# Optimization experiments

Measured on AMD Instinct MI355X. Metric: run time of the kernel, lower is better.

The kernel has to match this reference:

```python
import jax, jax.numpy as jnp
import numpy as np
from jax import lax

B, L, C = 4, 4096, 512
H = 8           # head_num
D = C // H      # head dim = 64
RR = 4          # reduction_ratio -> reducer conv kernel 7, stride 4
KS = 3          # MixFFN depthwise kernel
ER = 4          # expansion ratio -> 2048 channels
EPS = 1e-5      # torch LayerNorm default eps


def _ln(x, g, b):
    # LayerNorm over last axis, affine per-channel
    m = jnp.mean(x, axis=-1, keepdims=True)
    v = jnp.mean(jnp.square(x - m), axis=-1, keepdims=True)
    return (x - m) * lax.rsqrt(v + EPS) * g + b


def setup_inputs() -> dict:
    key = jax.random.key(0)
    ks = jax.random.split(key, 9)
    s = lambda fan: 1.0 / np.sqrt(fan)
    return {
        "x": jax.random.normal(ks[0], (B, L, C), jnp.float32),
        "w_q": jax.random.normal(ks[1], (C, C), jnp.float32) * s(C),
        "w_k": jax.random.normal(ks[2], (C, C), jnp.float32) * s(C),
        "w_v": jax.random.normal(ks[3], (C, C), jnp.float32) * s(C),
        "w_o": jax.random.normal(ks[4], (C, C), jnp.float32) * s(C),
        "w_red": jax.random.normal(ks[5], (C, C, 2 * RR - 1), jnp.float32) * s(C * (2 * RR - 1)),
        "w_ffn1": jax.random.normal(ks[6], (C, C), jnp.float32) * s(C),
        "w_ffn_dw": jax.random.normal(ks[7], (C * ER, 1, KS), jnp.float32) * s(KS),
        "w_ffn2": jax.random.normal(ks[8], (C, C * ER), jnp.float32) * s(C * ER),
        "ln_gamma": jnp.ones((6, C), jnp.float32),
        "ln_beta": jnp.zeros((6, C), jnp.float32),
    }


def reference(x, w_q, w_k, w_v, w_o, w_red, w_ffn1, w_ffn_dw, w_ffn2, ln_gamma, ln_beta):
    # ln indices: 0=ln1(pre-attn), 1=ln(reducer), 2=ln_q, 3=ln_k, 4=ln_v, 5=ln2(pre-ffn)
    residual = x
    h = _ln(x, ln_gamma[0], ln_beta[0])  # B L C

    # --- spatial-reduction for K/V: reflect-pad strided conv + LN ---
    p = (2 * RR - 1) // 2
    hr = jnp.transpose(h, (0, 2, 1))  # B C L
    hr = jnp.pad(hr, ((0, 0), (0, 0), (p, p)), mode="reflect")
    red = lax.conv_general_dilated(hr, w_red, window_strides=(RR,), padding="VALID",
                                   dimension_numbers=("NCH", "OIH", "NCH"))  # B C Lr
    red = jnp.transpose(red, (0, 2, 1))  # B Lr C
    red = _ln(red, ln_gamma[1], ln_beta[1])

    # --- QKV projections + LayerNorms ---
    q = _ln(h @ w_q.T, ln_gamma[2], ln_beta[2])      # B L C
    k = _ln(red @ w_k.T, ln_gamma[3], ln_beta[3])    # B Lr C
    v = _ln(red @ w_v.T, ln_gamma[4], ln_beta[4])    # B Lr C

    Lr = k.shape[1]
    q = q.reshape(B, L, H, D).transpose(0, 2, 1, 3)   # B h L d
    k = k.reshape(B, Lr, H, D).transpose(0, 2, 1, 3)  # B h Lr d
    v = v.reshape(B, Lr, H, D).transpose(0, 2, 1, 3)

    scores = jnp.einsum("bhqd,bhkd->bhqk", q, k) / jnp.sqrt(jnp.float32(D))
    attn = jax.nn.softmax(scores, axis=-1)
    out = jnp.einsum("bhqk,bhkd->bhqd", attn, v)
    out = out.transpose(0, 2, 1, 3).reshape(B, L, C)
    out = out @ w_o.T

    h2 = out + residual
    residual2 = h2
    f = _ln(h2, ln_gamma[5], ln_beta[5])  # B L C

    # --- MixFFN: 1x1 conv -> depthwise reflect conv (groups=C, out=ER*C) -> GELU -> 1x1 conv ---
    f = jnp.transpose(f, (0, 2, 1))  # B C L
    f = jnp.einsum("oi,bil->bol", w_ffn1, f)  # 1x1, C->C
    pk = (KS - 1) // 2
    fp = jnp.pad(f, ((0, 0), (0, 0), (pk, pk)), mode="reflect")
    f = lax.conv_general_dilated(fp, w_ffn_dw, window_strides=(1,), padding="VALID",
                                 dimension_numbers=("NCH", "OIH", "NCH"),
                                 feature_group_count=C)  # B (ER*C) L
    f = jax.nn.gelu(f, approximate=False)  # torch nn.GELU() is exact erf
    f = jnp.einsum("oi,bil->bol", w_ffn2, f)  # 1x1, ER*C->C
    f = jnp.transpose(f, (0, 2, 1))  # B L C

    return f + residual2
```

## Files before the change

kernel.cpp:

```cpp
#include <hip/hip_runtime.h>
#include <math.h>

typedef __attribute__((ext_vector_type(8))) short short8;
typedef __attribute__((ext_vector_type(4))) float f32x4;
typedef unsigned short u16;
typedef unsigned int u32;
typedef unsigned long long u64;

namespace {
constexpr int kB = 4;
constexpr int kL = 4096;
constexpr int kC = 512;
constexpr int kH = 8;
constexpr int kLr = 1024;
constexpr int kCH = 2048;
constexpr int kKred = 3584;
constexpr float kEps = 1e-5f;
}

#define WAIT_VM(n) asm volatile("s_waitcnt vmcnt(" #n ")" ::: "memory")
#define WAIT_LGKM0 asm volatile("s_waitcnt lgkmcnt(0)" ::: "memory")
#define BARRIER_SB() do { __builtin_amdgcn_s_barrier(); __builtin_amdgcn_sched_barrier(0); } while (0)

__device__ __forceinline__ float bf2f(u16 u) { return __uint_as_float(((u32)u) << 16); }
__device__ __forceinline__ u16 f2bf(float f) {
  u32 u = __float_as_uint(f);
  u32 r = (u + 0x7fffu + ((u >> 16) & 1u)) >> 16;
  return (u16)r;
}
__device__ __forceinline__ u32 cvtpk(float lo, float hi) {
  u32 r;
  asm("v_cvt_pk_bf16_f32 %0, %1, %2" : "=v"(r) : "v"(lo), "v"(hi));
  return r;
}

__device__ __forceinline__ void gload_lds16(const void* g, void* l) {
  __builtin_amdgcn_global_load_lds(
      (const __attribute__((address_space(1))) unsigned int*)g,
      (__attribute__((address_space(3))) unsigned int*)l, 16, 0, 0);
}

__device__ __forceinline__ short8 ldsfrag(const u16* base, int row, int col16) {
  return *(const short8*)(base + (size_t)(((row << 3) + (col16 ^ (row & 7))) << 3));
}

__global__ __launch_bounds__(256) void cvt_weights_kernel(
    const float* __restrict__ w_q, const float* __restrict__ w_k,
    const float* __restrict__ w_v, const float* __restrict__ w_o,
    const float* __restrict__ w_f1, const float* __restrict__ w_f2,
    u16* __restrict__ dst) {
  const int i = (blockIdx.x * 256 + threadIdx.x) * 4;
  const int seg = i >> 18;
  const float* src;
  int off;
  if (seg < 5) {
    src = (seg == 0) ? w_q : (seg == 1) ? w_k : (seg == 2) ? w_v : (seg == 3) ? w_o : w_f1;
    off = i & 262143;
  } else {
    src = w_f2;
    off = i - 1310720;
  }
  const float4 v = *(const float4*)(src + off);
  u16 o[4] = {f2bf(v.x), f2bf(v.y), f2bf(v.z), f2bf(v.w)};
  *(u64*)(dst + i) = *(u64*)o;
}

__global__ __launch_bounds__(256) void repack_wred_kernel(const float* __restrict__ src,
                                                          u16* __restrict__ dst) {
  const int idx = blockIdx.x * 256 + threadIdx.x;
  if (idx >= kC * kKred) return;
  const int o = idx / kKred;
  const int rem = idx - o * kKred;
  const int t = rem >> 9;
  const int i = rem & (kC - 1);
  dst[idx] = f2bf(src[(size_t)(o * kC + i) * 7 + t]);
}

__global__ __launch_bounds__(256) void ln_bf16_kernel(const float* __restrict__ in,
                                                      u16* __restrict__ out,
                                                      const float* __restrict__ g,
                                                      const float* __restrict__ be) {
  const int row = blockIdx.x;
  const int tid = threadIdx.x;
  const float2 v = *(const float2*)(in + (size_t)row * kC + tid * 2);
  float s = v.x + v.y;
  float ss = v.x * v.x + v.y * v.y;
#pragma unroll
  for (int off = 32; off > 0; off >>= 1) {
    s += __shfl_down(s, off);
    ss += __shfl_down(ss, off);
  }
  __shared__ float wsum[4][2];
  __shared__ float mi[2];
  const int wave = tid >> 6, lane = tid & 63;
  if (lane == 0) { wsum[wave][0] = s; wsum[wave][1] = ss; }
  __syncthreads();
  if (tid == 0) {
    const float S = wsum[0][0] + wsum[1][0] + wsum[2][0] + wsum[3][0];
    const float SS = wsum[0][1] + wsum[1][1] + wsum[2][1] + wsum[3][1];
    const float mean = S * (1.0f / kC);
    const float var = SS * (1.0f / kC) - mean * mean;
    mi[0] = mean;
    mi[1] = rsqrtf(var + kEps);
  }
  __syncthreads();
  const float mean = mi[0], inv = mi[1];
  const float2 gg = *(const float2*)(g + tid * 2);
  const float2 bb = *(const float2*)(be + tid * 2);
  u16 o2[2] = {f2bf((v.x - mean) * inv * gg.x + bb.x), f2bf((v.y - mean) * inv * gg.y + bb.y)};
  *(u32*)(out + (size_t)row * kC + tid * 2) = *(u32*)o2;
}

__global__ __launch_bounds__(256) void reduce2_ln_kernel(const float* __restrict__ P,
                                                         u16* __restrict__ out,
                                                         const float* __restrict__ g,
                                                         const float* __restrict__ be) {
  const int row = blockIdx.x;
  const int tid = threadIdx.x;
  const size_t stride = (size_t)kB * kLr * kC;
  float2 v = make_float2(0.f, 0.f);
#pragma unroll
  for (int z = 0; z < 2; ++z) {
    const float2 p = *(const float2*)(P + z * stride + (size_t)row * kC + tid * 2);
    v.x += p.x;
    v.y += p.y;
  }
  float s = v.x + v.y;
  float ss = v.x * v.x + v.y * v.y;
#pragma unroll
  for (int off = 32; off > 0; off >>= 1) {
    s += __shfl_down(s, off);
    ss += __shfl_down(ss, off);
  }
  __shared__ float wsum[4][2];
  __shared__ float mi[2];
  const int wave = tid >> 6, lane = tid & 63;
  if (lane == 0) { wsum[wave][0] = s; wsum[wave][1] = ss; }
  __syncthreads();
  if (tid == 0) {
    const float S = wsum[0][0] + wsum[1][0] + wsum[2][0] + wsum[3][0];
    const float SS = wsum[0][1] + wsum[1][1] + wsum[2][1] + wsum[3][1];
    const float mean = S * (1.0f / kC);
    const float var = SS * (1.0f / kC) - mean * mean;
    mi[0] = mean;
    mi[1] = rsqrtf(var + kEps);
  }
  __syncthreads();
  const float mean = mi[0], inv = mi[1];
  const float2 gg = *(const float2*)(g + tid * 2);
  const float2 bb = *(const float2*)(be + tid * 2);
  u16 o2[2] = {f2bf((v.x - mean) * inv * gg.x + bb.x), f2bf((v.y - mean) * inv * gg.y + bb.y)};
  *(u32*)(out + (size_t)row * kC + tid * 2) = *(u32*)o2;
}

__global__ __launch_bounds__(256) void dwgelu_kernel(const u16* __restrict__ f1,
                                                     const float* __restrict__ wdw,
                                                     u16* __restrict__ fdw) {
  const int row = blockIdx.x;
  const int l = row & (kL - 1);
  const int rb = row - l;
  const int cc0 = threadIdx.x * 8;
  const int cg = cc0 >> 2;
  const int lm = (l == 0) ? 1 : l - 1;
  const int lp = (l == kL - 1) ? kL - 2 : l + 1;
  const u32 xm = *(const u32*)(f1 + (size_t)(rb + lm) * kC + cg);
  const u32 x0 = *(const u32*)(f1 + (size_t)(rb + l) * kC + cg);
  const u32 xp = *(const u32*)(f1 + (size_t)(rb + lp) * kC + cg);
  const float xml = bf2f((u16)xm), xmh = bf2f((u16)(xm >> 16));
  const float x0l = bf2f((u16)x0), x0h = bf2f((u16)(x0 >> 16));
  const float xpl = bf2f((u16)xp), xph = bf2f((u16)(xp >> 16));
  float wv[24];
#pragma unroll
  for (int t = 0; t < 6; ++t)
    *(float4*)&wv[t * 4] = *(const float4*)(wdw + (size_t)cc0 * 3 + t * 4);
  short8 pk;
#pragma unroll
  for (int j = 0; j < 8; ++j) {
    const float a_ = (j < 4) ? xml : xmh;
    const float b_ = (j < 4) ? x0l : x0h;
    const float c_ = (j < 4) ? xpl : xph;
    const float dw = wv[j * 3] * a_ + wv[j * 3 + 1] * b_ + wv[j * 3 + 2] * c_;
    pk[j] = (short)f2bf(0.5f * dw * (1.0f + erff(dw * 0.70710678118654752440f)));
  }
  *(short8*)(fdw + (size_t)row * kCH + cc0) = pk;
}

__global__ __launch_bounds__(256) void mgemm_red_kernel(
    const u16* __restrict__ A, const u16* __restrict__ W, float* __restrict__ OutF,
    int M, int N, int K) {
  __shared__ __align__(16) u16 As[2][128 * 64];
  __shared__ __align__(16) u16 Bs[2][128 * 64];
  const int tid = threadIdx.x;
  const int lane = tid & 63, w = tid >> 6;
  const int m0 = blockIdx.y * 128, n0 = blockIdx.x * 128;
  const int wm = (w >> 1) * 64, wn = (w & 1) * 64;
  const f32x4 zero = {0.f, 0.f, 0.f, 0.f};
  f32x4 acc[4][4];
#pragma unroll
  for (int i = 0; i < 4; ++i)
#pragma unroll
    for (int j = 0; j < 4; ++j) acc[i][j] = zero;

  const int kc = K / gridDim.z;
  const int kBeg = blockIdx.z * kc;
  float* outp = OutF + (size_t)blockIdx.z * M * N;

  auto stage = [&](int buf, int k0) {
#pragma unroll
    for (int c = 0; c < 4; ++c) {
      const int ci = w * 4 + c;
      const int idx = ci * 64 + lane;
      const int row = idx >> 3, s = idx & 7;
      const int c16 = s ^ (row & 7);
      gload_lds16(W + (size_t)(n0 + row) * K + k0 + c16 * 8, (char*)Bs[buf] + ci * 1024);
      const int m = m0 + row;
      const int b = m >> 10, lr = m & (kLr - 1);
      const int k = k0 + c16 * 8;
      const int t = k >> 9, i = k & (kC - 1);
      int pos = 4 * lr + t - 3;
      pos = pos < 0 ? -pos : (pos >= kL ? 2 * kL - 2 - pos : pos);
      gload_lds16(A + ((size_t)(b << 12) + pos) * kC + i, (char*)As[buf] + ci * 1024);
    }
  };

  const int nk = kc >> 6;
  stage(0, kBeg);
  stage(1, kBeg + 64);
  for (int t = 0; t < nk; ++t) {
    const int cur = t & 1;
    if (t + 1 < nk) WAIT_VM(8); else WAIT_VM(0);
    BARRIER_SB();
#pragma unroll
    for (int kst = 0; kst < 2; ++kst) {
      short8 af[4], bfr[4];
      const int c16 = kst * 4 + (lane >> 4);
#pragma unroll
      for (int mb = 0; mb < 4; ++mb) af[mb] = ldsfrag(As[cur], wm + mb * 16 + (lane & 15), c16);
#pragma unroll
      for (int nb = 0; nb < 4; ++nb) bfr[nb] = ldsfrag(Bs[cur], wn + nb * 16 + (lane & 15), c16);
#pragma unroll
      for (int mb = 0; mb < 4; ++mb)
#pragma unroll
        for (int nb = 0; nb < 4; ++nb)
          acc[mb][nb] = __builtin_amdgcn_mfma_f32_16x16x32_bf16(af[mb], bfr[nb], acc[mb][nb], 0, 0, 0);
    }
    WAIT_LGKM0;
    BARRIER_SB();
    if (t + 2 < nk) stage(cur, kBeg + ((t + 2) << 6));
  }
#pragma unroll
  for (int mb = 0; mb < 4; ++mb)
#pragma unroll
    for (int r = 0; r < 4; ++r) {
      const int row = m0 + wm + mb * 16 + ((lane >> 4) << 2) + r;
#pragma unroll
      for (int nb = 0; nb < 4; ++nb)
        outp[(size_t)row * N + n0 + wn + nb * 16 + (lane & 15)] = acc[mb][nb][r];
    }
}

__global__ __launch_bounds__(256) void mgemm_res_kernel(
    const u16* __restrict__ A, const u16* __restrict__ W,
    const float* __restrict__ Res, float* __restrict__ OutF, int M, int N, int K) {
  __shared__ __align__(16) u16 As[2][128 * 64];
  __shared__ __align__(16) u16 Bs[2][128 * 64];
  const int tid = threadIdx.x;
  const int lane = tid & 63, w = tid >> 6;
  const int m0 = blockIdx.y * 128, n0 = blockIdx.x * 128;
  const int wm = (w >> 1) * 64, wn = (w & 1) * 64;
  const f32x4 zero = {0.f, 0.f, 0.f, 0.f};
  f32x4 acc[4][4];
#pragma unroll
  for (int i = 0; i < 4; ++i)
#pragma unroll
    for (int j = 0; j < 4; ++j) acc[i][j] = zero;

  auto stage = [&](int buf, int k0) {
#pragma unroll
    for (int c = 0; c < 4; ++c) {
      const int ci = w * 4 + c;
      const int idx = ci * 64 + lane;
      const int row = idx >> 3, s = idx & 7;
      const int c16 = s ^ (row & 7);
      gload_lds16(W + (size_t)(n0 + row) * K + k0 + c16 * 8, (char*)Bs[buf] + ci * 1024);
      gload_lds16(A + (size_t)(m0 + row) * K + k0 + c16 * 8, (char*)As[buf] + ci * 1024);
    }
  };

  const int nk = K >> 6;
  stage(0, 0);
  stage(1, 64);
  for (int t = 0; t < nk; ++t) {
    const int cur = t & 1;
    if (t + 1 < nk) WAIT_VM(8); else WAIT_VM(0);
    BARRIER_SB();
#pragma unroll
    for (int kst = 0; kst < 2; ++kst) {
      short8 af[4], bfr[4];
      const int c16 = kst * 4 + (lane >> 4);
#pragma unroll
      for (int mb = 0; mb < 4; ++mb) af[mb] = ldsfrag(As[cur], wm + mb * 16 + (lane & 15), c16);
#pragma unroll
      for (int nb = 0; nb < 4; ++nb) bfr[nb] = ldsfrag(Bs[cur], wn + nb * 16 + (lane & 15), c16);
#pragma unroll
      for (int mb = 0; mb < 4; ++mb)
#pragma unroll
        for (int nb = 0; nb < 4; ++nb)
          acc[mb][nb] = __builtin_amdgcn_mfma_f32_16x16x32_bf16(af[mb], bfr[nb], acc[mb][nb], 0, 0, 0);
    }
    WAIT_LGKM0;
    BARRIER_SB();
    if (t + 2 < nk) stage(cur, (t + 2) << 6);
  }
#pragma unroll
  for (int mb = 0; mb < 4; ++mb)
#pragma unroll
    for (int r = 0; r < 4; ++r) {
      const int row = m0 + wm + mb * 16 + ((lane >> 4) << 2) + r;
#pragma unroll
      for (int nb = 0; nb < 4; ++nb) {
        const size_t off = (size_t)row * N + n0 + wn + nb * 16 + (lane & 15);
        OutF[off] = acc[mb][nb][r] + Res[off];
      }
    }
}

template <int EPI>
__global__ __launch_bounds__(512) void gemm512_kernel(
    const u16* __restrict__ A, const u16* __restrict__ W,
    const float* __restrict__ Res, float* __restrict__ OutF,
    u16* __restrict__ OutB, u16* __restrict__ OutB2,
    int K, const float* __restrict__ gam, const float* __restrict__ bet, float oscale) {
  constexpr bool RES_ = (EPI == 3);
  constexpr bool LN_ = (EPI == 1 || EPI == 2 || EPI == 3);
  __shared__ __align__(16) u16 As[2][64 * 64];
  __shared__ __align__(16) u16 Bs[2][512 * 64];
  const int tid = threadIdx.x;
  const int lane = tid & 63, w = tid >> 6;
  const int l15 = lane & 15, g = lane >> 4;
  const int m0 = blockIdx.y * 64;
  const int n0 = blockIdx.x * 512;
  const int wn = w << 6;
  const f32x4 zero = {0.f, 0.f, 0.f, 0.f};
  f32x4 acc[4][4];
#pragma unroll
  for (int i = 0; i < 4; ++i)
#pragma unroll
    for (int j = 0; j < 4; ++j) acc[i][j] = zero;

  auto stage = [&](int buf, int k0) {
#pragma unroll
    for (int c = 0; c < 8; ++c) {
      const int cg = (w << 3) + c;
      const int idx = (cg << 6) + lane;
      const int row = idx >> 3, sl = idx & 7;
      const int c16 = sl ^ (row & 7);
      gload_lds16(W + (size_t)(n0 + row) * K + k0 + (c16 << 3), (char*)Bs[buf] + cg * 1024);
    }
    const int idx = (w << 6) + lane;
    const int row = idx >> 3, sl = idx & 7;
    const int c16 = sl ^ (row & 7);
    gload_lds16(A + (size_t)(m0 + row) * K + k0 + (c16 << 3), (char*)As[buf] + w * 1024);
  };

  const int nk = K >> 6;
  stage(0, 0);
  stage(1, 64);
  for (int t = 0; t < nk; ++t) {
    const int cur = t & 1;
    if (t + 1 < nk) WAIT_VM(9); else WAIT_VM(0);
    BARRIER_SB();
#pragma unroll
    for (int kst = 0; kst < 2; ++kst) {
      const int c16 = (kst << 2) + g;
      short8 af[4], bfr[4];
#pragma unroll
      for (int mb = 0; mb < 4; ++mb) af[mb] = ldsfrag(As[cur], (mb << 4) + l15, c16);
#pragma unroll
      for (int nb = 0; nb < 4; ++nb) bfr[nb] = ldsfrag(Bs[cur], wn + (nb << 4) + l15, c16);
#pragma unroll
      for (int mb = 0; mb < 4; ++mb)
#pragma unroll
        for (int nb = 0; nb < 4; ++nb)
          acc[mb][nb] = __builtin_amdgcn_mfma_f32_16x16x32_bf16(af[mb], bfr[nb], acc[mb][nb], 0, 0, 0);
    }
    WAIT_LGKM0;
    BARRIER_SB();
    if (t + 2 < nk) stage(cur, (t + 2) << 6);
  }

  if (RES_) {
#pragma unroll
    for (int mb = 0; mb < 4; ++mb)
#pragma unroll
      for (int r = 0; r < 4; ++r) {
        const int grow = m0 + (mb << 4) + (g << 2) + r;
#pragma unroll
        for (int nb = 0; nb < 4; ++nb)
          acc[mb][nb][r] += Res[(size_t)grow * kC + wn + (nb << 4) + l15];
      }
  }
  float* rs = (float*)As[0];
  float* rs2 = rs + 512;
  float2* minv = (float2*)(rs2 + 512);
  if (LN_) {
#pragma unroll
    for (int mb = 0; mb < 4; ++mb)
#pragma unroll
      for (int r = 0; r < 4; ++r) {
        float s = acc[mb][0][r] + acc[mb][1][r] + acc[mb][2][r] + acc[mb][3][r];
        float s2 = acc[mb][0][r] * acc[mb][0][r] + acc[mb][1][r] * acc[mb][1][r] +
                   acc[mb][2][r] * acc[mb][2][r] + acc[mb][3][r] * acc[mb][3][r];
        s += __shfl_xor(s, 1); s += __shfl_xor(s, 2); s += __shfl_xor(s, 4); s += __shfl_xor(s, 8);
        s2 += __shfl_xor(s2, 1); s2 += __shfl_xor(s2, 2); s2 += __shfl_xor(s2, 4); s2 += __shfl_xor(s2, 8);
        if (l15 == 0) {
          const int row = (mb << 4) + (g << 2) + r;
          rs[(w << 6) + row] = s;
          rs2[(w << 6) + row] = s2;
        }
      }
    __syncthreads();
    if (tid < 64) {
      float S = 0.f, SS = 0.f;
#pragma unroll
      for (int w8 = 0; w8 < 8; ++w8) { S += rs[(w8 << 6) + tid]; SS += rs2[(w8 << 6) + tid]; }
      const float mean = S * (1.0f / 512.0f);
      const float var = SS * (1.0f / 512.0f) - mean * mean;
      minv[tid] = make_float2(mean, rsqrtf(var + kEps));
    }
    __syncthreads();
  }
  float g4[4], b4[4];
  if (LN_) {
    const float* gp = (EPI == 2 && blockIdx.x) ? gam + kC : gam;
    const float* bp = (EPI == 2 && blockIdx.x) ? bet + kC : bet;
#pragma unroll
    for (int nb = 0; nb < 4; ++nb) {
      const int cc = wn + (nb << 4) + l15;
      g4[nb] = gp[cc];
      b4[nb] = bp[cc];
    }
  }
#pragma unroll
  for (int mb = 0; mb < 4; ++mb) {
#pragma unroll
    for (int r = 0; r < 4; ++r) {
      const int row = (mb << 4) + (g << 2) + r;
      const int grow = m0 + row;
      float2 mi = make_float2(0.f, 0.f);
      if (LN_) mi = minv[row];
#pragma unroll
      for (int nb = 0; nb < 4; ++nb) {
        const int cc = wn + (nb << 4) + l15;
        const float vv = acc[mb][nb][r];
        if (EPI == 0) {
          OutB[(size_t)grow * kC + cc] = f2bf(vv);
        } else if (EPI == 1) {
          OutB[(size_t)grow * kC + cc] = f2bf(((vv - mi.x) * mi.y * g4[nb] + b4[nb]) * oscale);
        } else if (EPI == 2) {
          const float lv = (vv - mi.x) * mi.y * g4[nb] + b4[nb];
          if (blockIdx.x == 0) {
            OutB[(size_t)grow * kC + cc] = f2bf(lv);
          } else {
            const int b = grow >> 10, lr = grow & (kLr - 1);
            const int hh = cc >> 6, d = cc & 63;
            OutB2[((size_t)((b << 3) + hh) * 64 + d) * kLr + lr] = f2bf(lv);
          }
        } else {
          OutF[(size_t)grow * kC + cc] = vv;
          OutB[(size_t)grow * kC + cc] = f2bf((vv - mi.x) * mi.y * g4[nb] + b4[nb]);
        }
      }
    }
  }
}

__global__ __launch_bounds__(256) void attn_mfma_kernel(
    const u16* __restrict__ q, const u16* __restrict__ k,
    const u16* __restrict__ vt, u16* __restrict__ o) {
  __shared__ __align__(16) u16 Ks[2][64 * 64];
  __shared__ __align__(16) u16 Vs[2][64 * 64];
  __shared__ __align__(16) u16 Ps[4][16 * 64];
  const int tid = threadIdx.x;
  const int lane = tid & 63, w = tid >> 6;
  const int qt = blockIdx.x, h = blockIdx.y, b = blockIdx.z;
  const int q0 = qt << 6;
  const int l15 = lane & 15, g = lane >> 4;

  short8 qf[2];
#pragma unroll
  for (int kst = 0; kst < 2; ++kst)
    qf[kst] = *(const short8*)(q + (size_t)((b << 12) + q0 + (w << 4) + l15) * kC +
                               (h << 6) + kst * 32 + g * 8);

  auto stageKV = [&](int buf, int t) {
    const int kv0 = t << 6;
#pragma unroll
    for (int c = 0; c < 2; ++c) {
      const int ci = (w << 1) + c;
      const int a16 = (ci << 6) + lane;
      const int r = a16 >> 3, sl = a16 & 7;
      const int c16 = sl ^ (r & 7);
      gload_lds16(k + (size_t)((b << 10) + kv0 + r) * kC + (h << 6) + (c16 << 3),
                  (char*)Ks[buf] + ci * 1024);
      gload_lds16(vt + (size_t)(((b << 3) + h) * 64 + r) * kLr + kv0 + (c16 << 3),
                  (char*)Vs[buf] + ci * 1024);
    }
  };

  stageKV(0, 0);
  stageKV(1, 1);

  const f32x4 zero = {0.f, 0.f, 0.f, 0.f};
  float m1 = -1e30f, l1 = 0.f;
  f32x4 accO[4] = {zero, zero, zero, zero};
  constexpr int nt = kLr / 64;

  for (int t = 0; t < nt; ++t) {
    const int cur = t & 1;
    if (t + 1 < nt) WAIT_VM(4); else WAIT_VM(0);
    BARRIER_SB();
    f32x4 st[4] = {zero, zero, zero, zero};
    __builtin_amdgcn_s_setprio(1);
#pragma unroll
    for (int kst = 0; kst < 2; ++kst) {
      const int c16 = (kst << 2) + g;
#pragma unroll
      for (int nb = 0; nb < 4; ++nb) {
        const short8 ak = ldsfrag(Ks[cur], (nb << 4) + l15, c16);
        st[nb] = __builtin_amdgcn_mfma_f32_16x16x32_bf16(ak, qf[kst], st[nb], 0, 0, 0);
      }
    }
    __builtin_amdgcn_s_setprio(0);
    {
      float pm = -1e30f;
#pragma unroll
      for (int nb = 0; nb < 4; ++nb)
#pragma unroll
        for (int r = 0; r < 4; ++r) pm = fmaxf(pm, st[nb][r]);
      pm = fmaxf(pm, __shfl_xor(pm, 16));
      pm = fmaxf(pm, __shfl_xor(pm, 32));
      const bool sk = __all(pm - m1 <= 11.5f);
      float scl = 1.0f;
      if (!sk) {
        const float mnew = fmaxf(m1, pm);
        scl = exp2f(m1 - mnew);
        m1 = mnew;
      }
      float ps = 0.f;
#pragma unroll
      for (int nb = 0; nb < 4; ++nb)
#pragma unroll
        for (int r = 0; r < 4; ++r) {
          const float e = exp2f(st[nb][r] - m1);
          st[nb][r] = e;
          ps += e;
        }
      ps += __shfl_xor(ps, 16);
      ps += __shfl_xor(ps, 32);
      l1 = l1 * scl + ps;
      char* pw = (char*)&Ps[w][0];
#pragma unroll
      for (int nb = 0; nb < 4; ++nb) {
        const u32 lo = cvtpk(st[nb][0], st[nb][1]);
        const u32 hi = cvtpk(st[nb][2], st[nb][3]);
        const int slot = ((nb << 1) + (g >> 1)) ^ (l15 & 7);
        *(u64*)(pw + (l15 << 7) + (slot << 4) + ((g & 1) << 3)) = ((u64)hi << 32) | lo;
      }
      if (!sk) {
        float scA[4];
#pragma unroll
        for (int r = 0; r < 4; ++r) scA[r] = __shfl(scl, (g << 2) + r);
#pragma unroll
        for (int d = 0; d < 4; ++d)
#pragma unroll
          for (int r = 0; r < 4; ++r) accO[d][r] *= scA[r];
      }
    }
    __builtin_amdgcn_s_setprio(1);
#pragma unroll
    for (int kvs = 0; kvs < 2; ++kvs) {
      const int c16 = (kvs << 2) + g;
      const short8 ap = ldsfrag(&Ps[w][0], l15, c16);
#pragma unroll
      for (int d = 0; d < 4; ++d) {
        const short8 bv = ldsfrag(Vs[cur], (d << 4) + l15, c16);
        accO[d] = __builtin_amdgcn_mfma_f32_16x16x32_bf16(ap, bv, accO[d], 0, 0, 0);
      }
    }
    __builtin_amdgcn_s_setprio(0);
    WAIT_LGKM0;
    BARRIER_SB();
    if (t + 2 < nt) stageKV(cur, t + 2);
  }
  float li[4];
#pragma unroll
  for (int r = 0; r < 4; ++r) li[r] = 1.0f / __shfl(l1, (g << 2) + r);
  const int qg = (b << 12) + q0 + (w << 4) + (g << 2);
#pragma unroll
  for (int d = 0; d < 4; ++d)
#pragma unroll
    for (int r = 0; r < 4; ++r)
      o[(size_t)(qg + r) * kC + (h << 6) + (d << 4) + l15] = f2bf(accO[d][r] * li[r]);
}

extern "C" void kernel_launch(void* const* d_in, const int* in_sizes, int n_in,
                              void* d_out, int out_size, void* d_ws, size_t ws_size,
                              hipStream_t stream) {
  const float* x      = (const float*)d_in[0];
  const float* w_q    = (const float*)d_in[1];
  const float* w_k    = (const float*)d_in[2];
  const float* w_v    = (const float*)d_in[3];
  const float* w_o    = (const float*)d_in[4];
  const float* w_red  = (const float*)d_in[5];
  const float* w_ffn1 = (const float*)d_in[6];
  const float* w_dw   = (const float*)d_in[7];
  const float* w_ffn2 = (const float*)d_in[8];
  const float* gam    = (const float*)d_in[9];
  const float* bet    = (const float*)d_in[10];
  float* out = (float*)d_out;

  const size_t nBLC = (size_t)kB * kL * kC;
  const size_t nBLrC = (size_t)kB * kLr * kC;
  u16* us = (u16*)d_ws;
  u16* wqb   = us;
  u16* wkb   = wqb + 262144;
  u16* wob   = wkb + 2 * 262144;
  u16* wf1b  = wob + 262144;
  u16* wf2b  = wf1b + 262144;
  u16* wredb = wf2b + 1048576;
  u16* h_b   = wredb + 1835008;
  u16* q_b   = h_b + nBLC;
  u16* red_b = q_b + nBLC;
  u16* k_b   = red_b + nBLrC;
  u16* vt_b  = k_b + nBLrC;
  float* S   = (float*)(vt_b + nBLrC);
  u16* fdw   = q_b;

  cvt_weights_kernel<<<2304, 256, 0, stream>>>(w_q, w_k, w_v, w_o, w_ffn1, w_ffn2, wqb);
  repack_wred_kernel<<<7168, 256, 0, stream>>>(w_red, wredb);

  ln_bf16_kernel<<<kB * kL, 256, 0, stream>>>(x, h_b, gam, bet);
  mgemm_red_kernel<<<dim3(4, 32, 2), 256, 0, stream>>>(h_b, wredb, S, kB * kLr, kC, kKred);
  reduce2_ln_kernel<<<kB * kLr, 256, 0, stream>>>(S, red_b, gam + kC, bet + kC);
  gemm512_kernel<1><<<dim3(1, 256), 512, 0, stream>>>(
      h_b, wqb, nullptr, nullptr, q_b, nullptr, kC, gam + 2 * kC, bet + 2 * kC,
      0.125f * 1.44269504088896f);
  gemm512_kernel<2><<<dim3(2, 64), 512, 0, stream>>>(
      red_b, wkb, nullptr, nullptr, k_b, vt_b, kC, gam + 3 * kC, bet + 3 * kC, 1.0f);
  attn_mfma_kernel<<<dim3(kL / 64, kH, kB), 256, 0, stream>>>(q_b, k_b, vt_b, h_b);
  gemm512_kernel<3><<<dim3(1, 256), 512, 0, stream>>>(
      h_b, wob, x, out, q_b, nullptr, kC, gam + 5 * kC, bet + 5 * kC, 1.0f);
  gemm512_kernel<0><<<dim3(1, 256), 512, 0, stream>>>(
      q_b, wf1b, nullptr, nullptr, h_b, nullptr, kC, nullptr, nullptr, 1.0f);
  dwgelu_kernel<<<kB * kL, 256, 0, stream>>>(h_b, w_dw, fdw);
  mgemm_res_kernel<<<dim3(4, 128), 256, 0, stream>>>(fdw, wf2b, out, out, kB * kL, kC, kCH);
}
```

Measured before the change: 319.8 us.

## Switch GEMM and attention kernels to 1024-thread blocks with single-stage prefetch

Replaces the explicit vmcnt-based two-stage prefetch with a simpler scheme: issue the next tile's loads, compute the current one, then __syncthreads. The 512-wide GEMM now uses 16 waves, splitting M across two wave rows, which halves per-wave accumulators. Attention grows to 16 waves and 256 queries per block, with K and V loads split across wave groups. This trades explicit wait control and prefetch depth for more waves per block and higher occupancy. The __syncthreads waits for all outstanding loads each step, so load latency may be less well hidden.

```diff
diff --git a/kernel.cpp b/kernel.cpp
--- a/kernel.cpp
+++ b/kernel.cpp
@@ -17,10 +17,6 @@
 constexpr int kKred = 3584;
 constexpr float kEps = 1e-5f;
 }
-
-#define WAIT_VM(n) asm volatile("s_waitcnt vmcnt(" #n ")" ::: "memory")
-#define WAIT_LGKM0 asm volatile("s_waitcnt lgkmcnt(0)" ::: "memory")
-#define BARRIER_SB() do { __builtin_amdgcn_s_barrier(); __builtin_amdgcn_sched_barrier(0); } while (0)
 
 __device__ __forceinline__ float bf2f(u16 u) { return __uint_as_float(((u32)u) << 16); }
 __device__ __forceinline__ u16 f2bf(float f) {
@@ -225,11 +221,10 @@
 
   const int nk = kc >> 6;
   stage(0, kBeg);
-  stage(1, kBeg + 64);
+  __syncthreads();
   for (int t = 0; t < nk; ++t) {
     const int cur = t & 1;
-    if (t + 1 < nk) WAIT_VM(8); else WAIT_VM(0);
-    BARRIER_SB();
+    if (t + 1 < nk) stage(cur ^ 1, kBeg + ((t + 1) << 6));
 #pragma unroll
     for (int kst = 0; kst < 2; ++kst) {
       short8 af[4], bfr[4];
@@ -244,9 +239,7 @@
         for (int nb = 0; nb < 4; ++nb)
           acc[mb][nb] = __builtin_amdgcn_mfma_f32_16x16x32_bf16(af[mb], bfr[nb], acc[mb][nb], 0, 0, 0);
     }
-    WAIT_LGKM0;
-    BARRIER_SB();
-    if (t + 2 < nk) stage(cur, kBeg + ((t + 2) << 6));
+    __syncthreads();
   }
 #pragma unroll
   for (int mb = 0; mb < 4; ++mb)
@@ -289,11 +282,10 @@
 
   const int nk = K >> 6;
   stage(0, 0);
-  stage(1, 64);
+  __syncthreads();
   for (int t = 0; t < nk; ++t) {
     const int cur = t & 1;
-    if (t + 1 < nk) WAIT_VM(8); else WAIT_VM(0);
-    BARRIER_SB();
+    if (t + 1 < nk) stage(cur ^ 1, (t + 1) << 6);
 #pragma unroll
     for (int kst = 0; kst < 2; ++kst) {
       short8 af[4], bfr[4];
@@ -308,9 +300,7 @@
         for (int nb = 0; nb < 4; ++nb)
           acc[mb][nb] = __builtin_amdgcn_mfma_f32_16x16x32_bf16(af[mb], bfr[nb], acc[mb][nb], 0, 0, 0);
     }
-    WAIT_LGKM0;
-    BARRIER_SB();
-    if (t + 2 < nk) stage(cur, (t + 2) << 6);
+    __syncthreads();
   }
 #pragma unroll
   for (int mb = 0; mb < 4; ++mb)
@@ -326,7 +316,7 @@
 }
 
 template <int EPI>
-__global__ __launch_bounds__(512) void gemm512_kernel(
+__global__ __launch_bounds__(1024) void gemm512_kernel(
     const u16* __restrict__ A, const u16* __restrict__ W,
     const float* __restrict__ Res, float* __restrict__ OutF,
     u16* __restrict__ OutB, u16* __restrict__ OutB2,
@@ -340,61 +330,61 @@
   const int l15 = lane & 15, g = lane >> 4;
   const int m0 = blockIdx.y * 64;
   const int n0 = blockIdx.x * 512;
-  const int wn = w << 6;
+  const int wm = (w >> 3) << 5;
+  const int wn = (w & 7) << 6;
   const f32x4 zero = {0.f, 0.f, 0.f, 0.f};
-  f32x4 acc[4][4];
-#pragma unroll
-  for (int i = 0; i < 4; ++i)
+  f32x4 acc[2][4];
+#pragma unroll
+  for (int i = 0; i < 2; ++i)
 #pragma unroll
     for (int j = 0; j < 4; ++j) acc[i][j] = zero;
 
   auto stage = [&](int buf, int k0) {
 #pragma unroll
-    for (int c = 0; c < 8; ++c) {
-      const int cg = (w << 3) + c;
+    for (int c = 0; c < 4; ++c) {
+      const int cg = (w << 2) + c;
       const int idx = (cg << 6) + lane;
       const int row = idx >> 3, sl = idx & 7;
       const int c16 = sl ^ (row & 7);
       gload_lds16(W + (size_t)(n0 + row) * K + k0 + (c16 << 3), (char*)Bs[buf] + cg * 1024);
     }
-    const int idx = (w << 6) + lane;
-    const int row = idx >> 3, sl = idx & 7;
-    const int c16 = sl ^ (row & 7);
-    gload_lds16(A + (size_t)(m0 + row) * K + k0 + (c16 << 3), (char*)As[buf] + w * 1024);
+    if (w < 8) {
+      const int idx = (w << 6) + lane;
+      const int row = idx >> 3, sl = idx & 7;
+      const int c16 = sl ^ (row & 7);
+      gload_lds16(A + (size_t)(m0 + row) * K + k0 + (c16 << 3), (char*)As[buf] + w * 1024);
+    }
   };
 
   const int nk = K >> 6;
   stage(0, 0);
-  stage(1, 64);
+  __syncthreads();
   for (int t = 0; t < nk; ++t) {
     const int cur = t & 1;
-    if (t + 1 < nk) WAIT_VM(9); else WAIT_VM(0);
-    BARRIER_SB();
+    if (t + 1 < nk) stage(cur ^ 1, (t + 1) << 6);
 #pragma unroll
     for (int kst = 0; kst < 2; ++kst) {
       const int c16 = (kst << 2) + g;
-      short8 af[4], bfr[4];
-#pragma unroll
-      for (int mb = 0; mb < 4; ++mb) af[mb] = ldsfrag(As[cur], (mb << 4) + l15, c16);
+      short8 af[2], bfr[4];
+#pragma unroll
+      for (int mb = 0; mb < 2; ++mb) af[mb] = ldsfrag(As[cur], wm + (mb << 4) + l15, c16);
 #pragma unroll
       for (int nb = 0; nb < 4; ++nb) bfr[nb] = ldsfrag(Bs[cur], wn + (nb << 4) + l15, c16);
 #pragma unroll
-      for (int mb = 0; mb < 4; ++mb)
+      for (int mb = 0; mb < 2; ++mb)
 #pragma unroll
         for (int nb = 0; nb < 4; ++nb)
           acc[mb][nb] = __builtin_amdgcn_mfma_f32_16x16x32_bf16(af[mb], bfr[nb], acc[mb][nb], 0, 0, 0);
     }
-    WAIT_LGKM0;
-    BARRIER_SB();
-    if (t + 2 < nk) stage(cur, (t + 2) << 6);
+    __syncthreads();
   }
 
   if (RES_) {
 #pragma unroll
-    for (int mb = 0; mb < 4; ++mb)
+    for (int mb = 0; mb < 2; ++mb)
 #pragma unroll
       for (int r = 0; r < 4; ++r) {
-        const int grow = m0 + (mb << 4) + (g << 2) + r;
+        const int grow = m0 + wm + (mb << 4) + (g << 2) + r;
 #pragma unroll
         for (int nb = 0; nb < 4; ++nb)
           acc[mb][nb][r] += Res[(size_t)grow * kC + wn + (nb << 4) + l15];
@@ -405,7 +395,7 @@
   float2* minv = (float2*)(rs2 + 512);
   if (LN_) {
 #pragma unroll
-    for (int mb = 0; mb < 4; ++mb)
+    for (int mb = 0; mb < 2; ++mb)
 #pragma unroll
       for (int r = 0; r < 4; ++r) {
         float s = acc[mb][0][r] + acc[mb][1][r] + acc[mb][2][r] + acc[mb][3][r];
@@ -414,16 +404,16 @@
         s += __shfl_xor(s, 1); s += __shfl_xor(s, 2); s += __shfl_xor(s, 4); s += __shfl_xor(s, 8);
         s2 += __shfl_xor(s2, 1); s2 += __shfl_xor(s2, 2); s2 += __shfl_xor(s2, 4); s2 += __shfl_xor(s2, 8);
         if (l15 == 0) {
-          const int row = (mb << 4) + (g << 2) + r;
-          rs[(w << 6) + row] = s;
-          rs2[(w << 6) + row] = s2;
+          const int rowf = wm + (mb << 4) + (g << 2) + r;
+          rs[((w & 7) << 6) + rowf] = s;
+          rs2[((w & 7) << 6) + rowf] = s2;
         }
       }
     __syncthreads();
     if (tid < 64) {
       float S = 0.f, SS = 0.f;
 #pragma unroll
-      for (int w8 = 0; w8 < 8; ++w8) { S += rs[(w8 << 6) + tid]; SS += rs2[(w8 << 6) + tid]; }
+      for (int c8 = 0; c8 < 8; ++c8) { S += rs[(c8 << 6) + tid]; SS += rs2[(c8 << 6) + tid]; }
       const float mean = S * (1.0f / 512.0f);
       const float var = SS * (1.0f / 512.0f) - mean * mean;
       minv[tid] = make_float2(mean, rsqrtf(var + kEps));
@@ -442,13 +432,13 @@
     }
   }
 #pragma unroll
-  for (int mb = 0; mb < 4; ++mb) {
+  for (int mb = 0; mb < 2; ++mb) {
 #pragma unroll
     for (int r = 0; r < 4; ++r) {
-      const int row = (mb << 4) + (g << 2) + r;
-      const int grow = m0 + row;
+      const int rowf = wm + (mb << 4) + (g << 2) + r;
+      const int grow = m0 + rowf;
       float2 mi = make_float2(0.f, 0.f);
-      if (LN_) mi = minv[row];
+      if (LN_) mi = minv[rowf];
 #pragma unroll
       for (int nb = 0; nb < 4; ++nb) {
         const int cc = wn + (nb << 4) + l15;
@@ -475,16 +465,16 @@
   }
 }
 
-__global__ __launch_bounds__(256) void attn_mfma_kernel(
+__global__ __launch_bounds__(1024) void attn_mfma_kernel(
     const u16* __restrict__ q, const u16* __restrict__ k,
     const u16* __restrict__ vt, u16* __restrict__ o) {
   __shared__ __align__(16) u16 Ks[2][64 * 64];
   __shared__ __align__(16) u16 Vs[2][64 * 64];
-  __shared__ __align__(16) u16 Ps[4][16 * 64];
+  __shared__ __align__(16) u16 Ps[16][16 * 64];
   const int tid = threadIdx.x;
   const int lane = tid & 63, w = tid >> 6;
   const int qt = blockIdx.x, h = blockIdx.y, b = blockIdx.z;
-  const int q0 = qt << 6;
+  const int q0 = qt << 8;
   const int l15 = lane & 15, g = lane >> 4;
 
   short8 qf[2];
@@ -495,31 +485,30 @@
 
   auto stageKV = [&](int buf, int t) {
     const int kv0 = t << 6;
-#pragma unroll
-    for (int c = 0; c < 2; ++c) {
-      const int ci = (w << 1) + c;
-      const int a16 = (ci << 6) + lane;
-      const int r = a16 >> 3, sl = a16 & 7;
-      const int c16 = sl ^ (r & 7);
+    const int ci = w & 7;
+    const int a16 = (ci << 6) + lane;
+    const int r = a16 >> 3, sl = a16 & 7;
+    const int c16 = sl ^ (r & 7);
+    if (w < 8)
       gload_lds16(k + (size_t)((b << 10) + kv0 + r) * kC + (h << 6) + (c16 << 3),
                   (char*)Ks[buf] + ci * 1024);
+    else
       gload_lds16(vt + (size_t)(((b << 3) + h) * 64 + r) * kLr + kv0 + (c16 << 3),
                   (char*)Vs[buf] + ci * 1024);
-    }
   };
 
   stageKV(0, 0);
-  stageKV(1, 1);
 
   const f32x4 zero = {0.f, 0.f, 0.f, 0.f};
   float m1 = -1e30f, l1 = 0.f;
   f32x4 accO[4] = {zero, zero, zero, zero};
   constexpr int nt = kLr / 64;
 
+  __syncthreads();
+
   for (int t = 0; t < nt; ++t) {
     const int cur = t & 1;
-    if (t + 1 < nt) WAIT_VM(4); else WAIT_VM(0);
-    BARRIER_SB();
+    if (t + 1 < nt) stageKV(cur ^ 1, t + 1);
     f32x4 st[4] = {zero, zero, zero, zero};
     __builtin_amdgcn_s_setprio(1);
 #pragma unroll
@@ -589,9 +578,7 @@
       }
     }
     __builtin_amdgcn_s_setprio(0);
-    WAIT_LGKM0;
-    BARRIER_SB();
-    if (t + 2 < nt) stageKV(cur, t + 2);
+    __syncthreads();
   }
   float li[4];
 #pragma unroll
@@ -643,15 +630,15 @@
   ln_bf16_kernel<<<kB * kL, 256, 0, stream>>>(x, h_b, gam, bet);
   mgemm_red_kernel<<<dim3(4, 32, 2), 256, 0, stream>>>(h_b, wredb, S, kB * kLr, kC, kKred);
   reduce2_ln_kernel<<<kB * kLr, 256, 0, stream>>>(S, red_b, gam + kC, bet + kC);
-  gemm512_kernel<1><<<dim3(1, 256), 512, 0, stream>>>(
+  gemm512_kernel<1><<<dim3(1, 256), 1024, 0, stream>>>(
       h_b, wqb, nullptr, nullptr, q_b, nullptr, kC, gam + 2 * kC, bet + 2 * kC,
       0.125f * 1.44269504088896f);
-  gemm512_kernel<2><<<dim3(2, 64), 512, 0, stream>>>(
+  gemm512_kernel<2><<<dim3(2, 64), 1024, 0, stream>>>(
       red_b, wkb, nullptr, nullptr, k_b, vt_b, kC, gam + 3 * kC, bet + 3 * kC, 1.0f);
-  attn_mfma_kernel<<<dim3(kL / 64, kH, kB), 256, 0, stream>>>(q_b, k_b, vt_b, h_b);
-  gemm512_kernel<3><<<dim3(1, 256), 512, 0, stream>>>(
+  attn_mfma_kernel<<<dim3(kL / 256, kH, kB), 1024, 0, stream>>>(q_b, k_b, vt_b, h_b);
+  gemm512_kernel<3><<<dim3(1, 256), 1024, 0, stream>>>(
       h_b, wob, x, out, q_b, nullptr, kC, gam + 5 * kC, bet + 5 * kC, 1.0f);
-  gemm512_kernel<0><<<dim3(1, 256), 512, 0, stream>>>(
+  gemm512_kernel<0><<<dim3(1, 256), 1024, 0, stream>>>(
       q_b, wf1b, nullptr, nullptr, h_b, nullptr, kC, nullptr, nullptr, 1.0f);
   dwgelu_kernel<<<kB * kL, 256, 0, stream>>>(h_b, w_dw, fdw);
   mgemm_res_kernel<<<dim3(4, 128), 256, 0, stream>>>(fdw, wf2b, out, out, kB * kL, kC, kCH);
```

New measurement: 302.8 us. 1.06x faster.
